# Kernel tuning notes

Measured on AMD Instinct MI355X. Metric: run time of the kernel, lower is better.

Reference implementation:

```python
import jax, jax.numpy as jnp
import numpy as np

BATCH = 128
SEQ_CTX = 64          # seq_len - 1 context steps
INPUT_SIZE = 320
OUTPUT_SIZE = 64
ITEM_DIM = INPUT_SIZE - OUTPUT_SIZE   # 256
HIDDEN = 1024
ONE_HOT = 192
BETA = 1.0


def setup_inputs() -> dict:
    key = jax.random.key(0)
    ks = jax.random.split(key, 6)
    return {
        "x_c": jax.random.normal(ks[0], (BATCH, SEQ_CTX, INPUT_SIZE), dtype=jnp.float32),
        "x_q": jax.random.normal(ks[1], (BATCH, ITEM_DIM), dtype=jnp.float32),
        "context_input": jax.random.uniform(ks[2], (BATCH, SEQ_CTX, ONE_HOT), dtype=jnp.float32),
        # W_hi initialized uniform(0, 0.5) as in the torch module
        "W_hi": jax.random.uniform(ks[3], (BATCH, HIDDEN, ITEM_DIM), dtype=jnp.float32) * 0.5,
        "W_oh": jax.random.uniform(ks[4], (BATCH, OUTPUT_SIZE, HIDDEN), dtype=jnp.float32),
        "W_reinst": jax.random.uniform(ks[5], (BATCH, HIDDEN, ONE_HOT), dtype=jnp.float32),
    }


def _context_scan(x_c, context_input, W_hi, W_oh, W_reinst):
    """Sequential one-winner Hebbian updates over the context sequence."""
    def step(carry, xs):
        W_hi, W_oh, W_reinst = carry
        x_curr, ctx = xs                              # (B, INPUT_SIZE), (B, ONE_HOT)
        x_item = x_curr[:, :ITEM_DIM]                 # (B, ITEM_DIM)
        x_label = x_curr[:, ITEM_DIM:]                # (B, OUTPUT_SIZE)
        logits = jnp.einsum('bhd,bd->bh', W_hi, x_item)
        # winner-take-all: one-hot of top-1 hidden unit (sparsify_tensor, k=1)
        z = jax.nn.one_hot(jnp.argmax(logits, axis=1), HIDDEN, dtype=W_hi.dtype)
        zc = z[:, :, None]                            # (B, H, 1)
        # W += z (x - W) : winner row overwritten with current pattern
        W_reinst = W_reinst + zc * (ctx[:, None, :] - W_reinst)
        W_hi = W_hi + zc * (x_item[:, None, :] - W_hi)
        W_oh = W_oh + z[:, None, :] * (x_label[:, :, None] - W_oh)
        return (W_hi, W_oh, W_reinst), None

    xs = (jnp.moveaxis(x_c, 1, 0), jnp.moveaxis(context_input, 1, 0))
    (W_hi, W_oh, W_reinst), _ = jax.lax.scan(step, (W_hi, W_oh, W_reinst), xs)
    return W_hi, W_oh, W_reinst


def reference(x_c, x_q, context_input, W_hi, W_oh, W_reinst):
    W_hi, W_oh, W_reinst = _context_scan(x_c, context_input, W_hi, W_oh, W_reinst)
    # query step
    logits = jnp.einsum('bhd,bd->bh', W_hi, x_q)          # (B, H)
    a = jax.nn.softmax(BETA * logits, axis=1)             # (B, H)
    out = jnp.einsum('boh,bh->bo', W_oh, a)               # (B, OUTPUT_SIZE)
    reinst_context = jnp.einsum('bhc,bh->bc', W_reinst, a)  # (B, ONE_HOT)
    return out, reinst_context
```

## Files before the change

kernel.cpp:

```cpp
#include <hip/hip_runtime.h>
#include <math.h>
#include <float.h>

#define BATCH 128
#define SEQ 64
#define IN 320
#define OUT 64
#define ITEM 256
#define HID 1024
#define OH 192
#define T65 65
#define KC 32
#define LDW 36

__device__ __forceinline__ void bett(float& bv, int& bh, float v, int h) {
  if (v > bv || (v == bv && h < bh)) { bv = v; bh = h; }
}

template<int R>
__device__ __forceinline__ void gemm_body(
    const float* __restrict__ wbase, int wstride, int wrows,
    const float* __restrict__ xcb, const float* __restrict__ xqb,
    float* __restrict__ Ws, float* __restrict__ Xs,
    int tid, int lane, float (&acc)[R][8], float (&accq)[R])
{
  const int rg = lane >> 3, cg = lane & 7;
  const int wv = tid >> 6;
  const int rowbase = wv * (8 * R);

  for (int kc = 0; kc < ITEM; kc += KC) {
    __syncthreads();
    const int nunit = wrows * (KC / 4);
    for (int u = tid; u < nunit; u += 256) {
      const int row = u >> 3, kq = (u & 7) << 2;
      const float4 v = *reinterpret_cast<const float4*>(wbase + (size_t)row * wstride + kc + kq);
      *reinterpret_cast<float4*>(&Ws[row * LDW + kq]) = v;
    }
    for (int u = tid; u < T65 * (KC / 4); u += 256) {
      const int row = u >> 3, kq = (u & 7) << 2;
      const float* src = (row < 64) ? (xcb + (size_t)row * IN) : xqb;
      const float4 v = *reinterpret_cast<const float4*>(src + kc + kq);
      *reinterpret_cast<float4*>(&Xs[row * LDW + kq]) = v;
    }
    __syncthreads();

    #pragma unroll
    for (int ks = 0; ks < KC; ks += 4) {
      float4 wf[R];
      #pragma unroll
      for (int i = 0; i < R; ++i)
        wf[i] = *reinterpret_cast<const float4*>(&Ws[(rowbase + rg + 8 * i) * LDW + ks]);
      const float4 qf = *reinterpret_cast<const float4*>(&Xs[64 * LDW + ks]);
      #pragma unroll
      for (int j = 0; j < 8; ++j) {
        const float4 xf = *reinterpret_cast<const float4*>(&Xs[(cg + 8 * j) * LDW + ks]);
        #pragma unroll
        for (int i = 0; i < R; ++i)
          acc[i][j] = fmaf(wf[i].w, xf.w, fmaf(wf[i].z, xf.z,
                      fmaf(wf[i].y, xf.y, fmaf(wf[i].x, xf.x, acc[i][j]))));
      }
      #pragma unroll
      for (int i = 0; i < R; ++i)
        accq[i] = fmaf(wf[i].w, qf.w, fmaf(wf[i].z, qf.z,
                  fmaf(wf[i].y, qf.y, fmaf(wf[i].x, qf.x, accq[i]))));
    }
  }
}

__global__ __launch_bounds__(256) void k_gemm(
    const float* __restrict__ W_hi, const float* __restrict__ x_c,
    const float* __restrict__ x_q, float* __restrict__ G, float* __restrict__ X)
{
  const int b = blockIdx.y, tile = blockIdx.x;
  const int tid = threadIdx.x, lane = tid & 63;
  const int rg = lane >> 3, cg = lane & 7, wv = tid >> 6;
  __shared__ float Ws[256 * LDW];
  __shared__ float Xs[T65 * LDW];
  const float* xcb = x_c + (size_t)b * SEQ * IN;
  const float* xqb = x_q + (size_t)b * ITEM;

  if (tile < 4) {
    float acc[8][8] = {}; float accq[8] = {};
    gemm_body<8>(W_hi + ((size_t)b * HID + tile * 256) * ITEM, ITEM, 256,
                 xcb, xqb, Ws, Xs, tid, lane, acc, accq);
    const int hb = tile * 256 + wv * 64 + rg;
    #pragma unroll
    for (int i = 0; i < 8; ++i) {
      const int h = hb + 8 * i;
      #pragma unroll
      for (int j = 0; j < 8; ++j)
        G[((size_t)b * T65 + (cg + 8 * j)) * HID + h] = acc[i][j];
      if (cg == 0) G[((size_t)b * T65 + 64) * HID + h] = accq[i];
    }
  } else {
    float acc[2][8] = {}; float accq[2] = {};
    gemm_body<2>(xcb, IN, 64, xcb, xqb, Ws, Xs, tid, lane, acc, accq);
    const int sb = wv * 16 + rg;
    #pragma unroll
    for (int i = 0; i < 2; ++i) {
      const int s = sb + 8 * i;
      #pragma unroll
      for (int j = 0; j < 8; ++j)
        X[((size_t)b * T65 + (cg + 8 * j)) * SEQ + s] = acc[i][j];
      if (cg == 0) X[((size_t)b * T65 + 64) * SEQ + s] = accq[i];
    }
  }
}

__global__ __launch_bounds__(64) void k_scan(
    const float* __restrict__ G, const float* __restrict__ X,
    float* __restrict__ a_mod, float* __restrict__ t_a)
{
  const int b = blockIdx.x, lane = threadIdx.x;
  __shared__ float Xs[T65 * SEQ];
  {
    const float4* Xsrc = reinterpret_cast<const float4*>(X + (size_t)b * T65 * SEQ);
    float4* Xd = reinterpret_cast<float4*>(Xs);
    for (int i = lane; i < T65 * SEQ / 4; i += 64) Xd[i] = Xsrc[i];
  }
  const float* Gb = G + (size_t)b * T65 * HID;
  float gcur[16];
  #pragma unroll
  for (int i = 0; i < 16; ++i) gcur[i] = Gb[lane + 64 * i];
  __syncthreads();

  unsigned vmask = 0xFFFFu;
  int myrow = 0x7FFFFFFF;
  bool active = false;

  for (int t = 0; t < SEQ; ++t) {
    const float* Gn = Gb + (size_t)(t + 1) * HID;
    float gnext[16];
    #pragma unroll
    for (int i = 0; i < 16; ++i) gnext[i] = Gn[lane + 64 * i];

    float bv = -FLT_MAX; int bh = 0x7FFFFFFF;
    #pragma unroll
    for (int i = 0; i < 16; ++i) {
      const float v = ((vmask >> i) & 1u) ? gcur[i] : -FLT_MAX;
      bett(bv, bh, v, lane + (i << 6));
    }
    {
      const float v = active ? Xs[t * SEQ + lane] : -FLT_MAX;
      bett(bv, bh, v, myrow);
    }
    #pragma unroll
    for (int m = 1; m < 64; m <<= 1) {
      const float ov = __shfl_xor(bv, m, 64);
      const int oh = __shfl_xor(bh, m, 64);
      bett(bv, bh, ov, oh);
    }
    if (active && myrow == bh) active = false;
    if (lane == t) { active = true; myrow = bh; }
    if ((bh & 63) == lane) vmask &= ~(1u << (bh >> 6));
    #pragma unroll
    for (int i = 0; i < 16; ++i) gcur[i] = gnext[i];
  }

  float e[16];
  float mx = -FLT_MAX;
  #pragma unroll
  for (int i = 0; i < 16; ++i) {
    e[i] = ((vmask >> i) & 1u) ? gcur[i] : -FLT_MAX;
    mx = fmaxf(mx, e[i]);
  }
  const float lt = active ? Xs[64 * SEQ + lane] : -FLT_MAX;
  mx = fmaxf(mx, lt);
  #pragma unroll
  for (int m = 1; m < 64; m <<= 1) mx = fmaxf(mx, __shfl_xor(mx, m, 64));
  float ssum = 0.f;
  #pragma unroll
  for (int i = 0; i < 16; ++i) {
    e[i] = ((vmask >> i) & 1u) ? expf(e[i] - mx) : 0.f;
    ssum += e[i];
  }
  const float et = active ? expf(lt - mx) : 0.f;
  ssum += et;
  #pragma unroll
  for (int m = 1; m < 64; m <<= 1) ssum += __shfl_xor(ssum, m, 64);
  const float inv = 1.f / ssum;
  #pragma unroll
  for (int i = 0; i < 16; ++i)
    a_mod[(size_t)b * HID + lane + 64 * i] = e[i] * inv;
  t_a[b * SEQ + lane] = et * inv;
}

__global__ __launch_bounds__(256) void k_partial(
    const float* __restrict__ W_oh, const float* __restrict__ W_re,
    const float* __restrict__ a_mod, float* __restrict__ p_out, float* __restrict__ p_re)
{
  const int b = blockIdx.y, p = blockIdx.x;
  const int tid = threadIdx.x;
  const int h0 = p * 256;
  __shared__ float as[256];
  as[tid] = a_mod[(size_t)b * HID + h0 + tid];
  __syncthreads();

  const int wv = tid >> 6, lane = tid & 63;
  if (wv < 3) {
    const int c = tid;
    const float* Wr = W_re + ((size_t)b * HID + h0) * OH + c;
    float acc = 0.f;
    #pragma unroll 8
    for (int h = 0; h < 256; ++h)
      acc = fmaf(Wr[(size_t)h * OH], as[h], acc);
    p_re[((size_t)b * 4 + p) * OH + c] = acc;
  } else {
    for (int o = 0; o < 64; ++o) {
      const float4 w4 = *reinterpret_cast<const float4*>(
          W_oh + ((size_t)b * OUT + o) * HID + h0 + lane * 4);
      const float* ap = &as[lane * 4];
      float acc = w4.x * ap[0] + w4.y * ap[1] + w4.z * ap[2] + w4.w * ap[3];
      #pragma unroll
      for (int m = 1; m < 64; m <<= 1) acc += __shfl_xor(acc, m, 64);
      if (lane == 0) p_out[((size_t)b * 4 + p) * OUT + o] = acc;
    }
  }
}

__global__ __launch_bounds__(256) void k_final(
    const float* __restrict__ x_c, const float* __restrict__ ctx,
    const float* __restrict__ p_out, const float* __restrict__ p_re,
    const float* __restrict__ t_a, float* __restrict__ out)
{
  const int b = blockIdx.x, tid = threadIdx.x;
  __shared__ float sa[SEQ];
  if (tid < SEQ) sa[tid] = t_a[b * SEQ + tid];
  __syncthreads();
  if (tid < OUT) {
    const int o = tid;
    float acc = 0.f;
    #pragma unroll
    for (int p = 0; p < 4; ++p) acc += p_out[((size_t)b * 4 + p) * OUT + o];
    for (int j = 0; j < SEQ; ++j) {
      const float w = sa[j];
      if (w != 0.f) acc = fmaf(x_c[((size_t)b * SEQ + j) * IN + ITEM + o], w, acc);
    }
    out[(size_t)b * OUT + o] = acc;
  } else if (tid < OUT + OH) {
    const int c = tid - OUT;
    float acc = 0.f;
    #pragma unroll
    for (int p = 0; p < 4; ++p) acc += p_re[((size_t)b * 4 + p) * OH + c];
    for (int j = 0; j < SEQ; ++j) {
      const float w = sa[j];
      if (w != 0.f) acc = fmaf(ctx[((size_t)b * SEQ + j) * OH + c], w, acc);
    }
    out[(size_t)BATCH * OUT + (size_t)b * OH + c] = acc;
  }
}

extern "C" void kernel_launch(void* const* d_in, const int* in_sizes, int n_in,
                              void* d_out, int out_size, void* d_ws, size_t ws_size,
                              hipStream_t stream)
{
  const float* x_c  = (const float*)d_in[0];
  const float* x_q  = (const float*)d_in[1];
  const float* ctx  = (const float*)d_in[2];
  const float* W_hi = (const float*)d_in[3];
  const float* W_oh = (const float*)d_in[4];
  const float* W_re = (const float*)d_in[5];

  char* ws = (char*)d_ws;
  float* G     = (float*)(ws);
  float* X     = (float*)(ws + 34078720);
  float* a_mod = (float*)(ws + 36208640);
  float* t_a   = (float*)(ws + 36732928);
  float* p_out = (float*)(ws + 36765696);
  float* p_re  = (float*)(ws + 36896768);

  k_gemm<<<dim3(5, BATCH), 256, 0, stream>>>(W_hi, x_c, x_q, G, X);
  k_scan<<<dim3(BATCH), 64, 0, stream>>>(G, X, a_mod, t_a);
  k_partial<<<dim3(4, BATCH), 256, 0, stream>>>(W_oh, W_re, a_mod, p_out, p_re);
  k_final<<<dim3(BATCH), 256, 0, stream>>>(x_c, ctx, p_out, p_re, t_a, (float*)d_out);
}
```

Measured before the change: 591.9 us.

## Deepen scan prefetch, template GEMM row counts, and tune unroll and launch bounds

The scan kernel now prefetches G rows two steps ahead instead of one, which hides more global-load latency on the serial argmax chain at the cost of 16 extra registers. The GEMM takes its weight row count as a template parameter so the tile-load loops fully unroll, and it sets a min-blocks-per-SM hint of 4 in launch bounds. The inner k loop drops from full unroll to unroll 2, and the reinstatement reduction unrolls 16 instead of 8. The occupancy hint may force register spills given the 8x8 accumulator tile.

```diff
diff --git a/kernel.cpp b/kernel.cpp
--- a/kernel.cpp
+++ b/kernel.cpp
@@ -17,9 +17,9 @@
   if (v > bv || (v == bv && h < bh)) { bv = v; bh = h; }
 }
 
-template<int R>
+template<int R, int WROWS>
 __device__ __forceinline__ void gemm_body(
-    const float* __restrict__ wbase, int wstride, int wrows,
+    const float* __restrict__ wbase, int wstride,
     const float* __restrict__ xcb, const float* __restrict__ xqb,
     float* __restrict__ Ws, float* __restrict__ Xs,
     int tid, int lane, float (&acc)[R][8], float (&accq)[R])
@@ -30,21 +30,26 @@
 
   for (int kc = 0; kc < ITEM; kc += KC) {
     __syncthreads();
-    const int nunit = wrows * (KC / 4);
-    for (int u = tid; u < nunit; u += 256) {
+    #pragma unroll
+    for (int u0 = 0; u0 < WROWS * (KC / 4); u0 += 256) {
+      const int u = u0 + tid;
       const int row = u >> 3, kq = (u & 7) << 2;
       const float4 v = *reinterpret_cast<const float4*>(wbase + (size_t)row * wstride + kc + kq);
       *reinterpret_cast<float4*>(&Ws[row * LDW + kq]) = v;
     }
-    for (int u = tid; u < T65 * (KC / 4); u += 256) {
-      const int row = u >> 3, kq = (u & 7) << 2;
-      const float* src = (row < 64) ? (xcb + (size_t)row * IN) : xqb;
-      const float4 v = *reinterpret_cast<const float4*>(src + kc + kq);
-      *reinterpret_cast<float4*>(&Xs[row * LDW + kq]) = v;
+    #pragma unroll
+    for (int u0 = 0; u0 < T65 * (KC / 4); u0 += 256) {
+      const int u = u0 + tid;
+      if (u < T65 * (KC / 4)) {
+        const int row = u >> 3, kq = (u & 7) << 2;
+        const float* src = (row < 64) ? (xcb + (size_t)row * IN) : xqb;
+        const float4 v = *reinterpret_cast<const float4*>(src + kc + kq);
+        *reinterpret_cast<float4*>(&Xs[row * LDW + kq]) = v;
+      }
     }
     __syncthreads();
 
-    #pragma unroll
+    #pragma unroll 2
     for (int ks = 0; ks < KC; ks += 4) {
       float4 wf[R];
       #pragma unroll
@@ -67,7 +72,7 @@
   }
 }
 
-__global__ __launch_bounds__(256) void k_gemm(
+__global__ __launch_bounds__(256, 4) void k_gemm(
     const float* __restrict__ W_hi, const float* __restrict__ x_c,
     const float* __restrict__ x_q, float* __restrict__ G, float* __restrict__ X)
 {
@@ -81,8 +86,8 @@
 
   if (tile < 4) {
     float acc[8][8] = {}; float accq[8] = {};
-    gemm_body<8>(W_hi + ((size_t)b * HID + tile * 256) * ITEM, ITEM, 256,
-                 xcb, xqb, Ws, Xs, tid, lane, acc, accq);
+    gemm_body<8, 256>(W_hi + ((size_t)b * HID + tile * 256) * ITEM, ITEM,
+                      xcb, xqb, Ws, Xs, tid, lane, acc, accq);
     const int hb = tile * 256 + wv * 64 + rg;
     #pragma unroll
     for (int i = 0; i < 8; ++i) {
@@ -94,7 +99,7 @@
     }
   } else {
     float acc[2][8] = {}; float accq[2] = {};
-    gemm_body<2>(xcb, IN, 64, xcb, xqb, Ws, Xs, tid, lane, acc, accq);
+    gemm_body<2, 64>(xcb, IN, xcb, xqb, Ws, Xs, tid, lane, acc, accq);
     const int sb = wv * 16 + rg;
     #pragma unroll
     for (int i = 0; i < 2; ++i) {
@@ -119,9 +124,11 @@
     for (int i = lane; i < T65 * SEQ / 4; i += 64) Xd[i] = Xsrc[i];
   }
   const float* Gb = G + (size_t)b * T65 * HID;
-  float gcur[16];
-  #pragma unroll
-  for (int i = 0; i < 16; ++i) gcur[i] = Gb[lane + 64 * i];
+  float g0[16], g1[16];
+  #pragma unroll
+  for (int i = 0; i < 16; ++i) g0[i] = Gb[lane + 64 * i];
+  #pragma unroll
+  for (int i = 0; i < 16; ++i) g1[i] = Gb[HID + lane + 64 * i];
   __syncthreads();
 
   unsigned vmask = 0xFFFFu;
@@ -129,15 +136,16 @@
   bool active = false;
 
   for (int t = 0; t < SEQ; ++t) {
-    const float* Gn = Gb + (size_t)(t + 1) * HID;
-    float gnext[16];
-    #pragma unroll
-    for (int i = 0; i < 16; ++i) gnext[i] = Gn[lane + 64 * i];
+    const int tn = (t + 2 < 64) ? (t + 2) : 64;
+    const float* Gn = Gb + (size_t)tn * HID;
+    float g2[16];
+    #pragma unroll
+    for (int i = 0; i < 16; ++i) g2[i] = Gn[lane + 64 * i];
 
     float bv = -FLT_MAX; int bh = 0x7FFFFFFF;
     #pragma unroll
     for (int i = 0; i < 16; ++i) {
-      const float v = ((vmask >> i) & 1u) ? gcur[i] : -FLT_MAX;
+      const float v = ((vmask >> i) & 1u) ? g0[i] : -FLT_MAX;
       bett(bv, bh, v, lane + (i << 6));
     }
     {
@@ -154,14 +162,14 @@
     if (lane == t) { active = true; myrow = bh; }
     if ((bh & 63) == lane) vmask &= ~(1u << (bh >> 6));
     #pragma unroll
-    for (int i = 0; i < 16; ++i) gcur[i] = gnext[i];
+    for (int i = 0; i < 16; ++i) { g0[i] = g1[i]; g1[i] = g2[i]; }
   }
 
   float e[16];
   float mx = -FLT_MAX;
   #pragma unroll
   for (int i = 0; i < 16; ++i) {
-    e[i] = ((vmask >> i) & 1u) ? gcur[i] : -FLT_MAX;
+    e[i] = ((vmask >> i) & 1u) ? g0[i] : -FLT_MAX;
     mx = fmaxf(mx, e[i]);
   }
   const float lt = active ? Xs[64 * SEQ + lane] : -FLT_MAX;
@@ -201,7 +209,7 @@
     const int c = tid;
     const float* Wr = W_re + ((size_t)b * HID + h0) * OH + c;
     float acc = 0.f;
-    #pragma unroll 8
+    #pragma unroll 16
     for (int h = 0; h < 256; ++h)
       acc = fmaf(Wr[(size_t)h * OH], as[h], acc);
     p_re[((size_t)b * 4 + p) * OH + c] = acc;
```

Result: faster. 500.7 us (-15.4%).
